# Performance work log

Hardware: AMD Instinct MI355X
Metric: run time of the kernel (lower is better)

## Reference

```python
import jax, jax.numpy as jnp
import numpy as np

B, N, D = 512, 256, 16   # batch, tokens (num_patches+1), embed_dim (= n_qubits)
STAGES = 4               # log2(D) butterfly stages


def _safe_acos(u):
    # matches torch acos + nan_to_num: out-of-range -> 0, with clean gradients
    ok = jnp.abs(u) <= 1.0
    return jnp.where(ok, jnp.arccos(jnp.clip(u, -1.0, 1.0)), 0.0)


def get_rbs_parameters(x):
    # x: [B, N, D] -> RBS angles [B, N, D-1]; recursive spherical-coordinate decomposition
    a0 = _safe_acos(x[..., 0])
    def step(carry, xi):
        t, a_prev = carry
        inv = jnp.nan_to_num(1.0 / jnp.sin(a_prev))
        t = t * inv
        a = _safe_acos(xi * t)
        return (t, a), a
    xs = jnp.moveaxis(x[..., 1:D - 1], -1, 0)  # [D-2, B, N]
    _, rest = jax.lax.scan(step, (jnp.ones_like(a0), a0), xs)
    alphas = jnp.concatenate([a0[None], rest], axis=0)  # [D-1, B, N]
    return jnp.moveaxis(alphas, 0, -1)


def amplitudes(alphas):
    # unary-state amplitudes prepared by the diagonal vector loader
    # a_i = cos(alpha_i) * prod_{k<i} sin(alpha_k);  a_{D-1} = prod_k sin(alpha_k)
    sins = jnp.sin(alphas)
    prefix = jnp.concatenate([jnp.ones_like(sins[..., :1]), jnp.cumprod(sins, axis=-1)], axis=-1)  # [B,N,D]
    return jnp.concatenate([prefix[..., :D - 1] * jnp.cos(alphas), prefix[..., D - 1:]], axis=-1)


def butterfly_matrix(angles):
    # orthogonal DxD matrix implemented by the Butterfly RBS circuit in the unary subspace
    d = 2 * angles.shape[1]
    M = jnp.eye(d, dtype=angles.dtype)
    for s in range(angles.shape[0]):
        step = 1 << s
        idx_i = np.array([i for i in range(d) if (i // step) % 2 == 0])
        idx_j = idx_i + step
        c = jnp.cos(angles[s])[:, None]
        sn = jnp.sin(angles[s])[:, None]
        Mi, Mj = M[idx_i], M[idx_j]
        M = M.at[idx_i].set(c * Mi + sn * Mj)
        M = M.at[idx_j].set(-sn * Mi + c * Mj)
    return M


def layer_norm(x, g, b, eps=1e-5):
    mu = jnp.mean(x, -1, keepdims=True)
    var = jnp.var(x, -1, keepdims=True)
    return (x - mu) / jnp.sqrt(var + eps) * g + b


def setup_inputs() -> dict:
    key = jax.random.key(0)
    ks = jax.random.split(key, 4)
    return {
        "x": jax.random.normal(ks[0], (B, N, D), jnp.float32),
        "ln1_g": jnp.ones((D,), jnp.float32),
        "ln1_b": jnp.zeros((D,), jnp.float32),
        "angles": jax.random.normal(ks[1], (STAGES, D // 2), jnp.float32),
        "ln2_g": jnp.ones((D,), jnp.float32),
        "ln2_b": jnp.zeros((D,), jnp.float32),
        "w1": jax.random.normal(ks[2], (D, 4 * D), jnp.float32) / np.sqrt(D).astype(np.float32),
        "b1": jnp.zeros((4 * D,), jnp.float32),
        "w2": jax.random.normal(ks[3], (4 * D, D), jnp.float32) / np.sqrt(4 * D).astype(np.float32),
        "b2": jnp.zeros((D,), jnp.float32),
    }


def reference(x, ln1_g, ln1_b, angles, ln2_g, ln2_b, w1, b1, w2, b2):
    inp = layer_norm(x, ln1_g, ln1_b) / 2.0
    alphas = jnp.nan_to_num(get_rbs_parameters(inp))
    a = amplitudes(alphas)                 # [B,N,D] loaded unary amplitudes
    W = butterfly_matrix(angles)           # [D,D] orthogonal butterfly
    Wa = jnp.einsum('de,bne->bnd', W, a)   # [B,N,D]
    vxT = jnp.abs(Wa)
    # xwx[b,i,j] = sqrt(P(qubit0=1)) = |<a_j| W |a_i>| for the xWx circuit
    xwx = jnp.abs(jnp.einsum('bid,bjd->bij', Wa, a))
    attn = jax.nn.softmax(xwx, axis=-1)
    x = x + jnp.einsum('bij,bjd->bid', attn, vxT)
    h = layer_norm(x, ln2_g, ln2_b)
    h = jax.nn.gelu(h @ w1 + b1, approximate=False) @ w2 + b2
    return x + h
```

## Files before the change

### kernel.cpp

```cpp
#include <hip/hip_runtime.h>
#include <math.h>

#define NTOK 256
#define DD 16
#define BDIM 512

typedef short short8 __attribute__((ext_vector_type(8)));
typedef float f32x16 __attribute__((ext_vector_type(16)));
typedef unsigned int u32;
typedef unsigned long long u64;

__device__ __forceinline__ u32 f2bf(float f) {
    u32 u = __float_as_uint(f);
    u += 0x7FFFu + ((u >> 16) & 1u);
    return u >> 16;
}
struct U128 { u64 a, b; };
__device__ __forceinline__ short8 ld8(const unsigned short* p) {
    U128 t;
    t.a = *(const u64*)(p);
    t.b = *(const u64*)(p + 4);
    return __builtin_bit_cast(short8, t);
}
__device__ __forceinline__ void pack_swap16(f32x16 p, short8& f0, short8& f1) {
    u32 W00, W01, W10, W11, W20, W21, W30, W31;
    asm("v_cvt_pk_bf16_f32 %0, %1, %2" : "=v"(W00) : "v"(p[0]),  "v"(p[1]));
    asm("v_cvt_pk_bf16_f32 %0, %1, %2" : "=v"(W01) : "v"(p[2]),  "v"(p[3]));
    asm("v_cvt_pk_bf16_f32 %0, %1, %2" : "=v"(W10) : "v"(p[4]),  "v"(p[5]));
    asm("v_cvt_pk_bf16_f32 %0, %1, %2" : "=v"(W11) : "v"(p[6]),  "v"(p[7]));
    asm("v_cvt_pk_bf16_f32 %0, %1, %2" : "=v"(W20) : "v"(p[8]),  "v"(p[9]));
    asm("v_cvt_pk_bf16_f32 %0, %1, %2" : "=v"(W21) : "v"(p[10]), "v"(p[11]));
    asm("v_cvt_pk_bf16_f32 %0, %1, %2" : "=v"(W30) : "v"(p[12]), "v"(p[13]));
    asm("v_cvt_pk_bf16_f32 %0, %1, %2" : "=v"(W31) : "v"(p[14]), "v"(p[15]));
    asm("v_permlane32_swap_b32 %0, %1" : "+v"(W00), "+v"(W10));
    asm("v_permlane32_swap_b32 %0, %1" : "+v"(W01), "+v"(W11));
    asm("v_permlane32_swap_b32 %0, %1" : "+v"(W20), "+v"(W30));
    asm("v_permlane32_swap_b32 %0, %1" : "+v"(W21), "+v"(W31));
    struct { u32 x, y, z, w; } i0{W00, W01, W10, W11}, i1{W20, W21, W30, W31};
    f0 = __builtin_bit_cast(short8, i0);
    f1 = __builtin_bit_cast(short8, i1);
}
__device__ __forceinline__ float gelu_erf(float v) {
    float xx = v * 0.70710678118654752f;
    float ax = fabsf(xx);
    float t = __builtin_amdgcn_rcpf(__builtin_fmaf(0.3275911f, ax, 1.0f));
    float poly = t * (0.254829592f + t * (-0.284496736f + t * (1.421413741f
               + t * (-1.453152027f + t * 1.061405429f))));
    float r = 1.0f - poly * __expf(-ax * ax);
    float e = copysignf(r, xx);
    return 0.5f * v * (1.0f + e);
}

__global__ __launch_bounds__(BDIM, 4) void qab_kernel(
    const float* __restrict__ x,
    const float* __restrict__ ln1_g, const float* __restrict__ ln1_b,
    const float* __restrict__ angles,
    const float* __restrict__ ln2_g, const float* __restrict__ ln2_b,
    const float* __restrict__ w1, const float* __restrict__ b1,
    const float* __restrict__ w2, const float* __restrict__ b2,
    float* __restrict__ out)
{
    __shared__ alignas(16) unsigned short a_bf[NTOK][20];
    __shared__ alignas(16) unsigned short wa_bf[NTOK][20];
    __shared__ alignas(16) unsigned short vxT[17][268];
    __shared__ alignas(16) unsigned short w1tb[64][20];
    __shared__ alignas(16) unsigned short w2tb[16][68];
    __shared__ alignas(16) float b1_lds[64];
    __shared__ alignas(16) float ln2g_lds[DD];
    __shared__ alignas(16) float ln2b_lds[DD];
    __shared__ alignas(16) float b2_lds[DD];

    const int b    = blockIdx.x;
    const int tid  = threadIdx.x;
    const int r    = tid & (NTOK - 1);
    const int q    = tid >> 8;
    const int w    = tid >> 6;
    const int l31  = tid & 31;
    const int hi   = (tid >> 5) & 1;
    const int lane = tid & 63;

    const float* xres = x + ((size_t)b * NTOK + 32 * w + l31) * DD;
    const float4 xra = *(const float4*)(xres + 4 * hi);
    const float4 xrb = *(const float4*)(xres + 8 + 4 * hi);

    f32x16 zc;
    #pragma unroll
    for (int t = 0; t < 16; ++t) zc[t] = 0.0f;

    float amp[DD];
    {
        const float* xrow = x + ((size_t)b * NTOK + r) * DD;
        float xr[DD];
        #pragma unroll
        for (int qq = 0; qq < 4; ++qq) {
            float4 v = ((const float4*)xrow)[qq];
            xr[4*qq+0] = v.x; xr[4*qq+1] = v.y; xr[4*qq+2] = v.z; xr[4*qq+3] = v.w;
        }
        float mu = 0.0f;
        #pragma unroll
        for (int d = 0; d < DD; ++d) mu += xr[d];
        mu *= (1.0f / DD);
        float var = 0.0f;
        #pragma unroll
        for (int d = 0; d < DD; ++d) { float dv = xr[d] - mu; var += dv * dv; }
        var *= (1.0f / DD);
        float rs = 1.0f / sqrtf(var + 1e-5f);
        float inp[DD];
        #pragma unroll
        for (int d = 0; d < DD; ++d)
            inp[d] = ((xr[d] - mu) * rs * ln1_g[d] + ln1_b[d]) * 0.5f;

        float P = 1.0f;
        #pragma unroll
        for (int i = 0; i < DD - 1; ++i) {
            float v = inp[i];
            float v2 = v * v;
            bool ok = v2 <= P;
            amp[i] = ok ? v : __builtin_amdgcn_sqrtf(P);
            P = ok ? __builtin_fmaf(-v, v, P) : 0.0f;
        }
        amp[DD - 1] = __builtin_amdgcn_sqrtf(P);
    }

    if (q == 0) {
        u32 aw[8];
        #pragma unroll
        for (int k = 0; k < 8; ++k)
            asm("v_cvt_pk_bf16_f32 %0, %1, %2" : "=v"(aw[k]) : "v"(amp[2*k]), "v"(amp[2*k+1]));
        *(u64*)&a_bf[r][0]  = (u64)aw[0] | ((u64)aw[1] << 32);
        *(u64*)&a_bf[r][4]  = (u64)aw[2] | ((u64)aw[3] << 32);
        *(u64*)&a_bf[r][8]  = (u64)aw[4] | ((u64)aw[5] << 32);
        *(u64*)&a_bf[r][12] = (u64)aw[6] | ((u64)aw[7] << 32);
        for (int i = r; i < 64 * DD; i += NTOK) {
            w1tb[i & 63][i >> 6] = (unsigned short)f2bf(w1[i]);
            w2tb[i & 15][i >> 4] = (unsigned short)f2bf(w2[i]);
        }
        if (r >= 128 && r < 192) b1_lds[r - 128] = b1[r - 128];
        if (r >= 192 && r < 208) ln2g_lds[r - 192] = ln2_g[r - 192];
        if (r >= 208 && r < 224) ln2b_lds[r - 208] = ln2_b[r - 208];
        if (r >= 224 && r < 240) b2_lds[r - 224] = b2[r - 224];
        vxT[16][r] = 0x3F80;
    } else {
        float sn_l = 0.0f, cs_l = 0.0f;
        if (lane < 32) __sincosf(angles[lane], &sn_l, &cs_l);
        #pragma unroll
        for (int s = 0; s < 4; ++s) {
            const int step = 1 << s;
            #pragma unroll
            for (int p = 0; p < 8; ++p) {
                const int i = ((p >> s) << (s + 1)) | (p & (step - 1));
                const int j = i + step;
                float sn = __shfl(sn_l, s * 8 + p, 64);
                float cs = __shfl(cs_l, s * 8 + p, 64);
                float vi = amp[i], vj = amp[j];
                amp[i] =  cs * vi + sn * vj;
                amp[j] = -sn * vi + cs * vj;
            }
        }
        u32 ww[8];
        #pragma unroll
        for (int k = 0; k < 8; ++k)
            asm("v_cvt_pk_bf16_f32 %0, %1, %2" : "=v"(ww[k]) : "v"(amp[2*k]), "v"(amp[2*k+1]));
        *(u64*)&wa_bf[r][0]  = (u64)ww[0] | ((u64)ww[1] << 32);
        *(u64*)&wa_bf[r][4]  = (u64)ww[2] | ((u64)ww[3] << 32);
        *(u64*)&wa_bf[r][8]  = (u64)ww[4] | ((u64)ww[5] << 32);
        *(u64*)&wa_bf[r][12] = (u64)ww[6] | ((u64)ww[7] << 32);
        #pragma unroll
        for (int d = 0; d < DD; ++d)
            vxT[d][r] = (unsigned short)f2bf(fabsf(amp[d]));
    }
    __syncthreads();

    const int ncl = (l31 < 16) ? l31 : 16;
    f32x16 Oacc = zc;
    {
        short8 waf = ld8(&wa_bf[w * 32 + l31][8 * hi]);
        #pragma unroll
        for (int jt = 0; jt < 8; ++jt) {
            short8 af = ld8(&a_bf[jt * 32 + l31][8 * hi]);
            f32x16 S = __builtin_amdgcn_mfma_f32_32x32x16_bf16(af, waf, zc, 0, 0, 0);
            f32x16 pv;
            #pragma unroll
            for (int t = 0; t < 16; ++t) pv[t] = __expf(fabsf(S[t]));
            short8 pb0, pb1;
            pack_swap16(pv, pb0, pb1);
            short8 va0 = ld8(&vxT[ncl][jt * 32 + 8 * hi]);
            short8 va1 = ld8(&vxT[ncl][jt * 32 + 16 + 8 * hi]);
            Oacc = __builtin_amdgcn_mfma_f32_32x32x16_bf16(va0, pb0, Oacc, 0, 0, 0);
            Oacc = __builtin_amdgcn_mfma_f32_32x32x16_bf16(va1, pb1, Oacc, 0, 0, 0);
        }
    }

    const float rl = 1.0f / Oacc[8];
    float o1[8];
    o1[0] = xra.x + Oacc[0] * rl;  o1[1] = xra.y + Oacc[1] * rl;
    o1[2] = xra.z + Oacc[2] * rl;  o1[3] = xra.w + Oacc[3] * rl;
    o1[4] = xrb.x + Oacc[4] * rl;  o1[5] = xrb.y + Oacc[5] * rl;
    o1[6] = xrb.z + Oacc[6] * rl;  o1[7] = xrb.w + Oacc[7] * rl;

    float s8 = 0.0f;
    #pragma unroll
    for (int t = 0; t < 8; ++t) s8 += o1[t];
    float mu2 = (s8 + __shfl_xor(s8, 32, 64)) * (1.0f / DD);
    float v8 = 0.0f;
    #pragma unroll
    for (int t = 0; t < 8; ++t) { float dv = o1[t] - mu2; v8 += dv * dv; }
    float var2 = (v8 + __shfl_xor(v8, 32, 64)) * (1.0f / DD);
    float rs2 = 1.0f / sqrtf(var2 + 1e-5f);

    const float4 g0v = *(const float4*)&ln2g_lds[4 * hi];
    const float4 g1v = *(const float4*)&ln2g_lds[8 + 4 * hi];
    const float4 bb0 = *(const float4*)&ln2b_lds[4 * hi];
    const float4 bb1 = *(const float4*)&ln2b_lds[8 + 4 * hi];
    float h[8];
    h[0] = (o1[0]-mu2)*rs2*g0v.x + bb0.x;  h[1] = (o1[1]-mu2)*rs2*g0v.y + bb0.y;
    h[2] = (o1[2]-mu2)*rs2*g0v.z + bb0.z;  h[3] = (o1[3]-mu2)*rs2*g0v.w + bb0.w;
    h[4] = (o1[4]-mu2)*rs2*g1v.x + bb1.x;  h[5] = (o1[5]-mu2)*rs2*g1v.y + bb1.y;
    h[6] = (o1[6]-mu2)*rs2*g1v.z + bb1.z;  h[7] = (o1[7]-mu2)*rs2*g1v.w + bb1.w;

    short8 hB;
    {
        u32 w0, w1u, w2u, w3;
        asm("v_cvt_pk_bf16_f32 %0, %1, %2" : "=v"(w0)  : "v"(h[0]), "v"(h[1]));
        asm("v_cvt_pk_bf16_f32 %0, %1, %2" : "=v"(w1u) : "v"(h[2]), "v"(h[3]));
        asm("v_cvt_pk_bf16_f32 %0, %1, %2" : "=v"(w2u) : "v"(h[4]), "v"(h[5]));
        asm("v_cvt_pk_bf16_f32 %0, %1, %2" : "=v"(w3)  : "v"(h[6]), "v"(h[7]));
        asm("s_nop 1\n\tv_permlane32_swap_b32 %0, %1" : "+v"(w0),  "+v"(w2u));
        asm("s_nop 1\n\tv_permlane32_swap_b32 %0, %1" : "+v"(w1u), "+v"(w3));
        struct { u32 x, y, z, w; } hw{w0, w1u, w2u, w3};
        hB = __builtin_bit_cast(short8, hw);
    }

    const int dcl = (l31 < 15) ? l31 : 15;
    f32x16 O2 = zc;
    {
        const float4 c0 = *(const float4*)&b2_lds[4 * hi];
        const float4 c1 = *(const float4*)&b2_lds[8 + 4 * hi];
        O2[0] = c0.x; O2[1] = c0.y; O2[2] = c0.z; O2[3] = c0.w;
        O2[4] = c1.x; O2[5] = c1.y; O2[6] = c1.z; O2[7] = c1.w;
    }
    #pragma unroll
    for (int kblk = 0; kblk < 2; ++kblk) {
        f32x16 Hc;
        {
            const float* bp = &b1_lds[32 * kblk];
            const float4 c0 = *(const float4*)(bp + 4 * hi);
            const float4 c1 = *(const float4*)(bp + 8 + 4 * hi);
            const float4 c2 = *(const float4*)(bp + 16 + 4 * hi);
            const float4 c3 = *(const float4*)(bp + 24 + 4 * hi);
            Hc[0]=c0.x; Hc[1]=c0.y; Hc[2]=c0.z; Hc[3]=c0.w;
            Hc[4]=c1.x; Hc[5]=c1.y; Hc[6]=c1.z; Hc[7]=c1.w;
            Hc[8]=c2.x; Hc[9]=c2.y; Hc[10]=c2.z; Hc[11]=c2.w;
            Hc[12]=c3.x; Hc[13]=c3.y; Hc[14]=c3.z; Hc[15]=c3.w;
        }
        short8 w1f = ld8(&w1tb[32 * kblk + l31][8 * hi]);
        f32x16 H = __builtin_amdgcn_mfma_f32_32x32x16_bf16(w1f, hB, Hc, 0, 0, 0);
        f32x16 gv;
        #pragma unroll
        for (int t = 0; t < 16; ++t) gv[t] = gelu_erf(H[t]);
        short8 gb0, gb1;
        pack_swap16(gv, gb0, gb1);
        short8 w2f0 = ld8(&w2tb[dcl][32 * kblk + 8 * hi]);
        short8 w2f1 = ld8(&w2tb[dcl][32 * kblk + 16 + 8 * hi]);
        O2 = __builtin_amdgcn_mfma_f32_32x32x16_bf16(w2f0, gb0, O2, 0, 0, 0);
        O2 = __builtin_amdgcn_mfma_f32_32x32x16_bf16(w2f1, gb1, O2, 0, 0, 0);
    }

    {
        float* orow = out + ((size_t)b * NTOK + 32 * w + l31) * DD;
        float4 oa, ob;
        oa.x = o1[0] + O2[0]; oa.y = o1[1] + O2[1];
        oa.z = o1[2] + O2[2]; oa.w = o1[3] + O2[3];
        ob.x = o1[4] + O2[4]; ob.y = o1[5] + O2[5];
        ob.z = o1[6] + O2[6]; ob.w = o1[7] + O2[7];
        *(float4*)(orow + 4 * hi) = oa;
        *(float4*)(orow + 8 + 4 * hi) = ob;
    }
}

extern "C" void kernel_launch(void* const* d_in, const int* in_sizes, int n_in,
                              void* d_out, int out_size, void* d_ws, size_t ws_size,
                              hipStream_t stream) {
    const float* x     = (const float*)d_in[0];
    const float* ln1_g = (const float*)d_in[1];
    const float* ln1_b = (const float*)d_in[2];
    const float* ang   = (const float*)d_in[3];
    const float* ln2_g = (const float*)d_in[4];
    const float* ln2_b = (const float*)d_in[5];
    const float* w1    = (const float*)d_in[6];
    const float* b1    = (const float*)d_in[7];
    const float* w2    = (const float*)d_in[8];
    const float* b2    = (const float*)d_in[9];
    float* out = (float*)d_out;

    const int B = in_sizes[0] / (NTOK * DD);
    hipLaunchKernelGGL(qab_kernel, dim3(B), dim3(BDIM), 0, stream,
                       x, ln1_g, ln1_b, ang, ln2_g, ln2_b, w1, b1, w2, b2, out);
}
```

Before: 20.21 us.

## Split each batch across two 256-thread blocks, recomputing shared prologue per block

Each batch is now processed by two blocks of 256 threads, each owning four 32-row query strips. Each block computes the full amplitude and butterfly prologue for all 256 tokens in one thread per token instead of splitting it across two thread halves, and also loads the weights itself. This doubles the grid to give more, smaller blocks for better occupancy and CU load balance. In exchange the prologue, including LayerNorm, the amplitude recursion, the butterfly and the weight conversion, is computed twice per batch, and each thread does the combined serial work.

```diff
diff --git a/kernel.cpp b/kernel.cpp
--- a/kernel.cpp
+++ b/kernel.cpp
@@ -3,7 +3,7 @@
 
 #define NTOK 256
 #define DD 16
-#define BDIM 512
+#define BDIM 256
 
 typedef short short8 __attribute__((ext_vector_type(8)));
 typedef float f32x16 __attribute__((ext_vector_type(16)));
@@ -70,16 +70,17 @@
     __shared__ alignas(16) float ln2b_lds[DD];
     __shared__ alignas(16) float b2_lds[DD];
 
-    const int b    = blockIdx.x;
-    const int tid  = threadIdx.x;
-    const int r    = tid & (NTOK - 1);
-    const int q    = tid >> 8;
-    const int w    = tid >> 6;
-    const int l31  = tid & 31;
-    const int hi   = (tid >> 5) & 1;
-    const int lane = tid & 63;
-
-    const float* xres = x + ((size_t)b * NTOK + 32 * w + l31) * DD;
+    const int b     = blockIdx.x >> 1;
+    const int half  = blockIdx.x & 1;
+    const int tid   = threadIdx.x;
+    const int r     = tid;
+    const int wv    = tid >> 6;
+    const int strip = half * 4 + wv;
+    const int l31   = tid & 31;
+    const int hi    = (tid >> 5) & 1;
+    const int lane  = tid & 63;
+
+    const float* xres = x + ((size_t)b * NTOK + 32 * strip + l31) * DD;
     const float4 xra = *(const float4*)(xres + 4 * hi);
     const float4 xrb = *(const float4*)(xres + 8 + 4 * hi);
 
@@ -122,7 +123,7 @@
         amp[DD - 1] = __builtin_amdgcn_sqrtf(P);
     }
 
-    if (q == 0) {
+    {
         u32 aw[8];
         #pragma unroll
         for (int k = 0; k < 8; ++k)
@@ -131,16 +132,9 @@
         *(u64*)&a_bf[r][4]  = (u64)aw[2] | ((u64)aw[3] << 32);
         *(u64*)&a_bf[r][8]  = (u64)aw[4] | ((u64)aw[5] << 32);
         *(u64*)&a_bf[r][12] = (u64)aw[6] | ((u64)aw[7] << 32);
-        for (int i = r; i < 64 * DD; i += NTOK) {
-            w1tb[i & 63][i >> 6] = (unsigned short)f2bf(w1[i]);
-            w2tb[i & 15][i >> 4] = (unsigned short)f2bf(w2[i]);
-        }
-        if (r >= 128 && r < 192) b1_lds[r - 128] = b1[r - 128];
-        if (r >= 192 && r < 208) ln2g_lds[r - 192] = ln2_g[r - 192];
-        if (r >= 208 && r < 224) ln2b_lds[r - 208] = ln2_b[r - 208];
-        if (r >= 224 && r < 240) b2_lds[r - 224] = b2[r - 224];
-        vxT[16][r] = 0x3F80;
-    } else {
+    }
+
+    {
         float sn_l = 0.0f, cs_l = 0.0f;
         if (lane < 32) __sincosf(angles[lane], &sn_l, &cs_l);
         #pragma unroll
@@ -169,12 +163,22 @@
         for (int d = 0; d < DD; ++d)
             vxT[d][r] = (unsigned short)f2bf(fabsf(amp[d]));
     }
+
+    for (int i = r; i < 64 * DD; i += BDIM) {
+        w1tb[i & 63][i >> 6] = (unsigned short)f2bf(w1[i]);
+        w2tb[i & 15][i >> 4] = (unsigned short)f2bf(w2[i]);
+    }
+    if (r < 64) b1_lds[r] = b1[r];
+    else if (r < 80)  ln2g_lds[r - 64] = ln2_g[r - 64];
+    else if (r < 96)  ln2b_lds[r - 80] = ln2_b[r - 80];
+    else if (r < 112) b2_lds[r - 96]  = b2[r - 96];
+    vxT[16][r] = 0x3F80;
     __syncthreads();
 
     const int ncl = (l31 < 16) ? l31 : 16;
     f32x16 Oacc = zc;
     {
-        short8 waf = ld8(&wa_bf[w * 32 + l31][8 * hi]);
+        short8 waf = ld8(&wa_bf[32 * strip + l31][8 * hi]);
         #pragma unroll
         for (int jt = 0; jt < 8; ++jt) {
             short8 af = ld8(&a_bf[jt * 32 + l31][8 * hi]);
@@ -267,7 +271,7 @@
     }
 
     {
-        float* orow = out + ((size_t)b * NTOK + 32 * w + l31) * DD;
+        float* orow = out + ((size_t)b * NTOK + 32 * strip + l31) * DD;
         float4 oa, ob;
         oa.x = o1[0] + O2[0]; oa.y = o1[1] + O2[1];
         oa.z = o1[2] + O2[2]; oa.w = o1[3] + O2[3];
@@ -294,6 +298,6 @@
     float* out = (float*)d_out;
 
     const int B = in_sizes[0] / (NTOK * DD);
-    hipLaunchKernelGGL(qab_kernel, dim3(B), dim3(BDIM), 0, stream,
+    hipLaunchKernelGGL(qab_kernel, dim3(2 * B), dim3(BDIM), 0, stream,
                        x, ln1_g, ln1_b, ang, ln2_g, ln2_b, w1, b1, w2, b2, out);
 }
```

Result: slower. 21.81 us (median of 2 runs) (+7.9%).

## Process two batches per 1024-thread block and fold log2e into exp2

Applied to the files above, without the earlier changes.

Each block now handles two batch elements with 1024 threads, so the grid is halved and per-batch LDS buffers are duplicated. Weight and bias staging into LDS is done once per block instead of once per batch, which amortizes the setup cost. Separately, Wa is pre-scaled by log2(e) before the bf16 conversion so the softmax exponent can use exp2f instead of __expf. The tradeoffs are fewer, larger blocks with a launch bound of 8, which may limit occupancy and scheduling flexibility, and a slight change in bf16 rounding of the scores.

```diff
diff --git a/kernel.cpp b/kernel.cpp
--- a/kernel.cpp
+++ b/kernel.cpp
@@ -3,7 +3,7 @@
 
 #define NTOK 256
 #define DD 16
-#define BDIM 512
+#define BDIM 1024
 
 typedef short short8 __attribute__((ext_vector_type(8)));
 typedef float f32x16 __attribute__((ext_vector_type(16)));
@@ -51,7 +51,7 @@
     return 0.5f * v * (1.0f + e);
 }
 
-__global__ __launch_bounds__(BDIM, 4) void qab_kernel(
+__global__ __launch_bounds__(BDIM, 8) void qab_kernel(
     const float* __restrict__ x,
     const float* __restrict__ ln1_g, const float* __restrict__ ln1_b,
     const float* __restrict__ angles,
@@ -60,9 +60,9 @@
     const float* __restrict__ w2, const float* __restrict__ b2,
     float* __restrict__ out)
 {
-    __shared__ alignas(16) unsigned short a_bf[NTOK][20];
-    __shared__ alignas(16) unsigned short wa_bf[NTOK][20];
-    __shared__ alignas(16) unsigned short vxT[17][268];
+    __shared__ alignas(16) unsigned short a_bf[2][NTOK][20];
+    __shared__ alignas(16) unsigned short wa_bf[2][NTOK][20];
+    __shared__ alignas(16) unsigned short vxT[2][17][268];
     __shared__ alignas(16) unsigned short w1tb[64][20];
     __shared__ alignas(16) unsigned short w2tb[16][68];
     __shared__ alignas(16) float b1_lds[64];
@@ -70,16 +70,18 @@
     __shared__ alignas(16) float ln2b_lds[DD];
     __shared__ alignas(16) float b2_lds[DD];
 
-    const int b    = blockIdx.x;
     const int tid  = threadIdx.x;
-    const int r    = tid & (NTOK - 1);
-    const int q    = tid >> 8;
-    const int w    = tid >> 6;
+    const int h    = tid >> 9;
+    const int b    = blockIdx.x * 2 + h;
+    const int tl   = tid & 511;
+    const int r    = tl & (NTOK - 1);
+    const int q    = tl >> 8;
+    const int wl   = tl >> 6;
     const int l31  = tid & 31;
     const int hi   = (tid >> 5) & 1;
     const int lane = tid & 63;
 
-    const float* xres = x + ((size_t)b * NTOK + 32 * w + l31) * DD;
+    const float* xres = x + ((size_t)b * NTOK + 32 * wl + l31) * DD;
     const float4 xra = *(const float4*)(xres + 4 * hi);
     const float4 xrb = *(const float4*)(xres + 8 + 4 * hi);
 
@@ -127,19 +129,21 @@
         #pragma unroll
         for (int k = 0; k < 8; ++k)
             asm("v_cvt_pk_bf16_f32 %0, %1, %2" : "=v"(aw[k]) : "v"(amp[2*k]), "v"(amp[2*k+1]));
-        *(u64*)&a_bf[r][0]  = (u64)aw[0] | ((u64)aw[1] << 32);
-        *(u64*)&a_bf[r][4]  = (u64)aw[2] | ((u64)aw[3] << 32);
-        *(u64*)&a_bf[r][8]  = (u64)aw[4] | ((u64)aw[5] << 32);
-        *(u64*)&a_bf[r][12] = (u64)aw[6] | ((u64)aw[7] << 32);
-        for (int i = r; i < 64 * DD; i += NTOK) {
-            w1tb[i & 63][i >> 6] = (unsigned short)f2bf(w1[i]);
-            w2tb[i & 15][i >> 4] = (unsigned short)f2bf(w2[i]);
-        }
-        if (r >= 128 && r < 192) b1_lds[r - 128] = b1[r - 128];
-        if (r >= 192 && r < 208) ln2g_lds[r - 192] = ln2_g[r - 192];
-        if (r >= 208 && r < 224) ln2b_lds[r - 208] = ln2_b[r - 208];
-        if (r >= 224 && r < 240) b2_lds[r - 224] = b2[r - 224];
-        vxT[16][r] = 0x3F80;
+        *(u64*)&a_bf[h][r][0]  = (u64)aw[0] | ((u64)aw[1] << 32);
+        *(u64*)&a_bf[h][r][4]  = (u64)aw[2] | ((u64)aw[3] << 32);
+        *(u64*)&a_bf[h][r][8]  = (u64)aw[4] | ((u64)aw[5] << 32);
+        *(u64*)&a_bf[h][r][12] = (u64)aw[6] | ((u64)aw[7] << 32);
+        if (h == 0) {
+            for (int i = r; i < 64 * DD; i += NTOK) {
+                w1tb[i & 63][i >> 6] = (unsigned short)f2bf(w1[i]);
+                w2tb[i & 15][i >> 4] = (unsigned short)f2bf(w2[i]);
+            }
+            if (r >= 128 && r < 192) b1_lds[r - 128] = b1[r - 128];
+            if (r >= 192 && r < 208) ln2g_lds[r - 192] = ln2_g[r - 192];
+            if (r >= 208 && r < 224) ln2b_lds[r - 208] = ln2_b[r - 208];
+            if (r >= 224 && r < 240) b2_lds[r - 224] = b2[r - 224];
+        }
+        vxT[h][16][r] = 0x3F80;
     } else {
         float sn_l = 0.0f, cs_l = 0.0f;
         if (lane < 32) __sincosf(angles[lane], &sn_l, &cs_l);
@@ -157,35 +161,37 @@
                 amp[j] = -sn * vi + cs * vj;
             }
         }
+        const float L2E = 1.4426950408889634f;
         u32 ww[8];
         #pragma unroll
         for (int k = 0; k < 8; ++k)
-            asm("v_cvt_pk_bf16_f32 %0, %1, %2" : "=v"(ww[k]) : "v"(amp[2*k]), "v"(amp[2*k+1]));
-        *(u64*)&wa_bf[r][0]  = (u64)ww[0] | ((u64)ww[1] << 32);
-        *(u64*)&wa_bf[r][4]  = (u64)ww[2] | ((u64)ww[3] << 32);
-        *(u64*)&wa_bf[r][8]  = (u64)ww[4] | ((u64)ww[5] << 32);
-        *(u64*)&wa_bf[r][12] = (u64)ww[6] | ((u64)ww[7] << 32);
+            asm("v_cvt_pk_bf16_f32 %0, %1, %2" : "=v"(ww[k])
+                : "v"(amp[2*k] * L2E), "v"(amp[2*k+1] * L2E));
+        *(u64*)&wa_bf[h][r][0]  = (u64)ww[0] | ((u64)ww[1] << 32);
+        *(u64*)&wa_bf[h][r][4]  = (u64)ww[2] | ((u64)ww[3] << 32);
+        *(u64*)&wa_bf[h][r][8]  = (u64)ww[4] | ((u64)ww[5] << 32);
+        *(u64*)&wa_bf[h][r][12] = (u64)ww[6] | ((u64)ww[7] << 32);
         #pragma unroll
         for (int d = 0; d < DD; ++d)
-            vxT[d][r] = (unsigned short)f2bf(fabsf(amp[d]));
+            vxT[h][d][r] = (unsigned short)f2bf(fabsf(amp[d]));
     }
     __syncthreads();
 
     const int ncl = (l31 < 16) ? l31 : 16;
     f32x16 Oacc = zc;
     {
-        short8 waf = ld8(&wa_bf[w * 32 + l31][8 * hi]);
+        short8 waf = ld8(&wa_bf[h][32 * wl + l31][8 * hi]);
         #pragma unroll
         for (int jt = 0; jt < 8; ++jt) {
-            short8 af = ld8(&a_bf[jt * 32 + l31][8 * hi]);
+            short8 af = ld8(&a_bf[h][jt * 32 + l31][8 * hi]);
             f32x16 S = __builtin_amdgcn_mfma_f32_32x32x16_bf16(af, waf, zc, 0, 0, 0);
             f32x16 pv;
             #pragma unroll
-            for (int t = 0; t < 16; ++t) pv[t] = __expf(fabsf(S[t]));
+            for (int t = 0; t < 16; ++t) pv[t] = exp2f(fabsf(S[t]));
             short8 pb0, pb1;
             pack_swap16(pv, pb0, pb1);
-            short8 va0 = ld8(&vxT[ncl][jt * 32 + 8 * hi]);
-            short8 va1 = ld8(&vxT[ncl][jt * 32 + 16 + 8 * hi]);
+            short8 va0 = ld8(&vxT[h][ncl][jt * 32 + 8 * hi]);
+            short8 va1 = ld8(&vxT[h][ncl][jt * 32 + 16 + 8 * hi]);
             Oacc = __builtin_amdgcn_mfma_f32_32x32x16_bf16(va0, pb0, Oacc, 0, 0, 0);
             Oacc = __builtin_amdgcn_mfma_f32_32x32x16_bf16(va1, pb1, Oacc, 0, 0, 0);
         }
@@ -212,19 +218,19 @@
     const float4 g1v = *(const float4*)&ln2g_lds[8 + 4 * hi];
     const float4 bb0 = *(const float4*)&ln2b_lds[4 * hi];
     const float4 bb1 = *(const float4*)&ln2b_lds[8 + 4 * hi];
-    float h[8];
-    h[0] = (o1[0]-mu2)*rs2*g0v.x + bb0.x;  h[1] = (o1[1]-mu2)*rs2*g0v.y + bb0.y;
-    h[2] = (o1[2]-mu2)*rs2*g0v.z + bb0.z;  h[3] = (o1[3]-mu2)*rs2*g0v.w + bb0.w;
-    h[4] = (o1[4]-mu2)*rs2*g1v.x + bb1.x;  h[5] = (o1[5]-mu2)*rs2*g1v.y + bb1.y;
-    h[6] = (o1[6]-mu2)*rs2*g1v.z + bb1.z;  h[7] = (o1[7]-mu2)*rs2*g1v.w + bb1.w;
+    float hv[8];
+    hv[0] = (o1[0]-mu2)*rs2*g0v.x + bb0.x;  hv[1] = (o1[1]-mu2)*rs2*g0v.y + bb0.y;
+    hv[2] = (o1[2]-mu2)*rs2*g0v.z + bb0.z;  hv[3] = (o1[3]-mu2)*rs2*g0v.w + bb0.w;
+    hv[4] = (o1[4]-mu2)*rs2*g1v.x + bb1.x;  hv[5] = (o1[5]-mu2)*rs2*g1v.y + bb1.y;
+    hv[6] = (o1[6]-mu2)*rs2*g1v.z + bb1.z;  hv[7] = (o1[7]-mu2)*rs2*g1v.w + bb1.w;
 
     short8 hB;
     {
         u32 w0, w1u, w2u, w3;
-        asm("v_cvt_pk_bf16_f32 %0, %1, %2" : "=v"(w0)  : "v"(h[0]), "v"(h[1]));
-        asm("v_cvt_pk_bf16_f32 %0, %1, %2" : "=v"(w1u) : "v"(h[2]), "v"(h[3]));
-        asm("v_cvt_pk_bf16_f32 %0, %1, %2" : "=v"(w2u) : "v"(h[4]), "v"(h[5]));
-        asm("v_cvt_pk_bf16_f32 %0, %1, %2" : "=v"(w3)  : "v"(h[6]), "v"(h[7]));
+        asm("v_cvt_pk_bf16_f32 %0, %1, %2" : "=v"(w0)  : "v"(hv[0]), "v"(hv[1]));
+        asm("v_cvt_pk_bf16_f32 %0, %1, %2" : "=v"(w1u) : "v"(hv[2]), "v"(hv[3]));
+        asm("v_cvt_pk_bf16_f32 %0, %1, %2" : "=v"(w2u) : "v"(hv[4]), "v"(hv[5]));
+        asm("v_cvt_pk_bf16_f32 %0, %1, %2" : "=v"(w3)  : "v"(hv[6]), "v"(hv[7]));
         asm("s_nop 1\n\tv_permlane32_swap_b32 %0, %1" : "+v"(w0),  "+v"(w2u));
         asm("s_nop 1\n\tv_permlane32_swap_b32 %0, %1" : "+v"(w1u), "+v"(w3));
         struct { u32 x, y, z, w; } hw{w0, w1u, w2u, w3};
@@ -267,7 +273,7 @@
     }
 
     {
-        float* orow = out + ((size_t)b * NTOK + 32 * w + l31) * DD;
+        float* orow = out + ((size_t)b * NTOK + 32 * wl + l31) * DD;
         float4 oa, ob;
         oa.x = o1[0] + O2[0]; oa.y = o1[1] + O2[1];
         oa.z = o1[2] + O2[2]; oa.w = o1[3] + O2[3];
@@ -294,6 +300,6 @@
     float* out = (float*)d_out;
 
     const int B = in_sizes[0] / (NTOK * DD);
-    hipLaunchKernelGGL(qab_kernel, dim3(B), dim3(BDIM), 0, stream,
+    hipLaunchKernelGGL(qab_kernel, dim3(B / 2), dim3(BDIM), 0, stream,
                        x, ln1_g, ln1_b, ang, ln2_g, ln2_b, w1, b1, w2, b2, out);
 }
```

Result: slower. 24.31 us (+20.2%).
